# Kernel tuning notes

Measured on AMD Instinct MI355X. Metric: run time of the kernel, lower is better.

The kernel has to match this reference:

```python
import jax, jax.numpy as jnp
import numpy as np

N_NODES = 50000
N_EDGES = 500000
D_IN = 128
D_HID = 128
C = 1.0          # curvature (same for every layer)
MIN_NORM = 1e-15
MAX_TANH_ARG = 15.0
PROJ_EPS = 4e-3  # float32 boundary eps used by hgcn PoincareBall.proj


def _artanh(x):
    x = jnp.clip(x, -1.0 + 1e-7, 1.0 - 1e-7)
    return 0.5 * (jnp.log1p(x) - jnp.log1p(-x))


def _tanh(x):
    return jnp.tanh(jnp.clip(x, -MAX_TANH_ARG, MAX_TANH_ARG))


def _norm(x):
    return jnp.maximum(jnp.linalg.norm(x, axis=-1, keepdims=True), MIN_NORM)


def proj(x, c):
    # clip points to stay strictly inside the Poincare ball
    n = _norm(x)
    maxnorm = (1.0 - PROJ_EPS) / jnp.sqrt(c)
    return jnp.where(n > maxnorm, x / n * maxnorm, x)


def expmap0(u, c):
    sc = jnp.sqrt(c)
    n = _norm(u)
    return _tanh(sc * n) * u / (sc * n)


def logmap0(p, c):
    sc = jnp.sqrt(c)
    n = _norm(p)
    return _artanh(sc * n) * p / (sc * n)


def mobius_add(x, y, c):
    x2 = jnp.sum(x * x, -1, keepdims=True)
    y2 = jnp.sum(y * y, -1, keepdims=True)
    xy = jnp.sum(x * y, -1, keepdims=True)
    num = (1.0 + 2.0 * c * xy + c * y2) * x + (1.0 - c * x2) * y
    den = 1.0 + 2.0 * c * xy + c * c * x2 * y2
    return num / jnp.maximum(den, MIN_NORM)


def mobius_matvec(m, x, c):
    sc = jnp.sqrt(c)
    xn = _norm(x)
    mx = x @ m.T                                   # [N, out]
    mxn = _norm(mx)
    res = _tanh(mxn / xn * _artanh(sc * xn)) * mx / (mxn * sc)
    is_zero = jnp.all(mx == 0.0, axis=-1, keepdims=True)
    return jnp.where(is_zero, jnp.zeros_like(res), res)


def hyp_linear(x, W, b, c):
    h = proj(mobius_matvec(W, x, c), c)
    hyp_bias = proj(expmap0(b[None, :], c), c)     # proj_tan0 is identity on the ball
    return proj(mobius_add(h, hyp_bias, c), c)


def hyp_agg(x, src, dst, edge_weight, c):
    x_tan = logmap0(x, c)                          # [N, d] tangent at origin
    msg = edge_weight[:, None] * x_tan[src]        # [E, d] gather + scale
    agg = jax.ops.segment_sum(msg, dst, num_segments=N_NODES)  # spmm(adj, x_tan)
    return proj(expmap0(agg, c), c)


def hyp_act(x, c_in, c_out):
    xt = jax.nn.relu(logmap0(x, c_in))
    return proj(expmap0(xt, c_out), c_out)


def setup_inputs() -> dict:
    key = jax.random.key(0)
    ks = jax.random.split(key, 8)
    x = jax.random.normal(ks[0], (N_NODES, D_IN), dtype=jnp.float32) * 0.1
    src = jax.random.randint(ks[1], (N_EDGES,), 0, N_NODES)
    dst = jax.random.randint(ks[2], (N_EDGES,), 0, N_NODES)
    edge_weight = jax.random.uniform(ks[3], (N_EDGES,), dtype=jnp.float32) * 0.1
    s1 = 1.0 / np.sqrt(D_IN)
    W1 = jax.random.normal(ks[4], (D_HID, D_IN), dtype=jnp.float32) * s1
    b1 = jax.random.normal(ks[5], (D_HID,), dtype=jnp.float32) * 0.01
    W2 = jax.random.normal(ks[6], (D_HID, D_HID), dtype=jnp.float32) * s1
    b2 = jax.random.normal(ks[7], (D_HID,), dtype=jnp.float32) * 0.01
    return {"x": x, "src": src, "dst": dst, "edge_weight": edge_weight,
            "W1": W1, "b1": b1, "W2": W2, "b2": b2}


def reference(x, src, dst, edge_weight, W1, b1, W2, b2):
    c = jnp.float32(C)
    # HGCN.encode: proj_tan0 (identity for PoincareBall) -> expmap0 -> proj
    h = proj(expmap0(x, c), c)
    # layer 1: HypLinear -> HypAgg -> HypAct
    h = hyp_linear(h, W1, b1, c)
    h = hyp_agg(h, src, dst, edge_weight, c)
    h = hyp_act(h, c, c)
    # layer 2
    h = hyp_linear(h, W2, b2, c)
    h = hyp_agg(h, src, dst, edge_weight, c)
    h = hyp_act(h, c, c)
    return h
```

## Files before the change

### kernel.cpp

```cpp
#include <hip/hip_runtime.h>
#include <math.h>

#define MIN_NORM 1e-15f
#define MAXNORM  0.996f
#define ARTANH_CLIP 0.99999988f

typedef __bf16 bf16x8 __attribute__((ext_vector_type(8)));
typedef float  f32x4  __attribute__((ext_vector_type(4)));

union FragU { ushort u[8]; uint4 q; bf16x8 v; };

__device__ __forceinline__ float wave_sum(float v) {
#pragma unroll
    for (int off = 32; off > 0; off >>= 1) v += __shfl_xor(v, off, 64);
    return v;
}

__device__ __forceinline__ float artanh_c(float x) {
    x = fminf(fmaxf(x, -ARTANH_CLIP), ARTANH_CLIP);
    return 0.5f * (log1pf(x) - log1pf(-x));
}

__device__ __forceinline__ float tanh_c(float x) {
    return tanhf(fminf(fmaxf(x, -15.f), 15.f));
}

__device__ __forceinline__ float proj_factor(float n2) {
    float n = fmaxf(sqrtf(n2), MIN_NORM);
    return (n > MAXNORM) ? (MAXNORM / n) : 1.f;
}

__device__ __forceinline__ unsigned short f2bf(float f) {
    unsigned u = __float_as_uint(f);
    return (unsigned short)((u + 0x7fffu + ((u >> 16) & 1u)) >> 16);
}
__device__ __forceinline__ float bf2f(unsigned short h) {
    return __uint_as_float((unsigned)h << 16);
}
__device__ __forceinline__ float bflo(unsigned u) { return __uint_as_float(u << 16); }
__device__ __forceinline__ float bfhi(unsigned u) { return __uint_as_float(u & 0xffff0000u); }

__device__ __forceinline__ void red16_f4(float4& v) {
#pragma unroll
    for (int off = 1; off < 16; off <<= 1) {
        v.x += __shfl_xor(v.x, off, 64);
        v.y += __shfl_xor(v.y, off, 64);
        v.z += __shfl_xor(v.z, off, 64);
        v.w += __shfl_xor(v.w, off, 64);
    }
}

__device__ __forceinline__ float bcast_row(const float4& v, int r) {
    const int src = (r >> 2) << 4;
    const float a = __shfl(v.x, src, 64);
    const float b = __shfl(v.y, src, 64);
    const float c = __shfl(v.z, src, 64);
    const float d = __shfl(v.w, src, 64);
    const float lo = (r & 1) ? b : a;
    const float hi = (r & 1) ? d : c;
    return (r & 2) ? hi : lo;
}

__device__ __forceinline__ void pack_w4(const float4 w4, int o, int k, char* out) {
    ushort4 h, l;
    h.x = f2bf(w4.x); l.x = f2bf(w4.x - bf2f(h.x));
    h.y = f2bf(w4.y); l.y = f2bf(w4.y - bf2f(h.y));
    h.z = f2bf(w4.z); l.z = f2bf(w4.z - bf2f(h.z));
    h.w = f2bf(w4.w); l.w = f2bf(w4.w - bf2f(h.w));
    const int prow = ((o & 7) << 4) | (o >> 3);
    const unsigned byte = (unsigned)((prow << 8) + (k << 1)) ^ (unsigned)((prow & 7) << 4);
    *reinterpret_cast<ushort4*>(out + byte) = h;
    *reinterpret_cast<ushort4*>(out + 32768 + byte) = l;
}

__global__ __launch_bounds__(256)
void setup_kernel(const float* __restrict__ W1, const float* __restrict__ W2,
                  char* __restrict__ g1, char* __restrict__ g2,
                  const float* __restrict__ b1, const float* __restrict__ b2,
                  float* __restrict__ hb1, float* __restrict__ hb2,
                  const int* __restrict__ dst, int* __restrict__ cnt, int E) {
    const int b = blockIdx.x;
    if (b < 32) {
        const float* W = (b < 16) ? W1 : W2;
        char* out = (b < 16) ? g1 : g2;
        const int i = (((b & 15) * 256) + threadIdx.x) * 4;
        pack_w4(*reinterpret_cast<const float4*>(&W[i]), i >> 7, i & 127, out);
    } else if (b == 32) {
        if (threadIdx.x < 64) {
            const int lane = threadIdx.x;
#pragma unroll
            for (int j = 0; j < 2; ++j) {
                const float* bb = j ? b2 : b1;
                float* hb = j ? hb2 : hb1;
                float v0 = bb[lane], v1 = bb[lane + 64];
                float n2 = wave_sum(v0 * v0 + v1 * v1);
                float n = fmaxf(sqrtf(n2), MIN_NORM);
                float sc = tanh_c(n) / n;
                sc *= proj_factor(sc * sc * n2);
                hb[lane] = v0 * sc;
                hb[lane + 64] = v1 * sc;
            }
        }
    } else {
        const int e = (b - 33) * 256 + threadIdx.x;
        if (e < E) atomicAdd(&cnt[dst[e]], 1);
    }
}


__global__ void scan1(const int* __restrict__ cnt, int* __restrict__ ptr,
                      int* __restrict__ bsum, int N) {
    __shared__ int s[256];
    const int t = threadIdx.x;
    const int i = blockIdx.x * 256 + t;
    int v = (i < N) ? cnt[i] : 0;
    s[t] = v;
    __syncthreads();
#pragma unroll
    for (int off = 1; off < 256; off <<= 1) {
        int add = (t >= off) ? s[t - off] : 0;
        __syncthreads();
        s[t] += add;
        __syncthreads();
    }
    if (i < N) ptr[i] = s[t] - v;
    if (t == 255) bsum[blockIdx.x] = s[255];
}

__global__ void scan2(const int* __restrict__ bsum, int* __restrict__ bscan, int nb) {
    __shared__ int s[256];
    const int t = threadIdx.x;
    int v = (t < nb) ? bsum[t] : 0;
    s[t] = v;
    __syncthreads();
#pragma unroll
    for (int off = 1; off < 256; off <<= 1) {
        int add = (t >= off) ? s[t - off] : 0;
        __syncthreads();
        s[t] += add;
        __syncthreads();
    }
    bscan[t] = s[t] - v;
}

__global__ void scan3(const int* __restrict__ bscan, int* __restrict__ ptr,
                      int* __restrict__ cursor, int N, int E) {
    const int i = blockIdx.x * blockDim.x + threadIdx.x;
    if (i < N) {
        const int p = ptr[i] + bscan[i >> 8];
        ptr[i] = p;
        cursor[i] = p;
    }
    if (i == 0) ptr[N] = E;
}

__global__ void scatter_kernel(const int* __restrict__ src, const int* __restrict__ dst,
                               const float* __restrict__ ew, int* __restrict__ cursor,
                               unsigned* __restrict__ epk, int E) {
    int e = blockIdx.x * blockDim.x + threadIdx.x;
    if (e >= E) return;
    int pos = atomicAdd(&cursor[dst[e]], 1);
    epk[pos] = ((unsigned)src[e] << 16) | (unsigned)f2bf(ew[e]);
}

template <bool PRELUDE, bool BF16IN, bool BF16OUT>
__global__ __launch_bounds__(1024, 4)
void hyp_linear_tan_mfma(const void* __restrict__ xin, const char* __restrict__ gWpack,
                         const float* __restrict__ hb, void* __restrict__ xtan,
                         int n_rows) {
    __shared__ __align__(16) char sW[65536];

    const int tid = threadIdx.x;
    const int lane = tid & 63, wid = tid >> 6;
    const int r15 = lane & 15, g = lane >> 4;

    const int tiles = (n_rows + 15) >> 4;
    const int tile = blockIdx.x + gridDim.x * wid;
    const bool active = (tile < tiles);
    const int rowbase = tile << 4;
    const int myrow = rowbase + r15;
    const bool rok = active && (myrow < n_rows);

    float4 xa[4], xb[4];
    uint4 xu[4];
    if (BF16IN) {
        const char* xr = (const char*)xin + (size_t)myrow * 256 + g * 16;
#pragma unroll
        for (int kc = 0; kc < 4; ++kc)
            xu[kc] = rok ? *reinterpret_cast<const uint4*>(xr + kc * 64)
                         : make_uint4(0u, 0u, 0u, 0u);
    } else {
        const float* xr = (const float*)xin + (size_t)myrow * 128 + g * 8;
#pragma unroll
        for (int kc = 0; kc < 4; ++kc) {
            if (rok) {
                xa[kc] = *reinterpret_cast<const float4*>(xr + kc * 32);
                xb[kc] = *reinterpret_cast<const float4*>(xr + kc * 32 + 4);
            } else {
                xa[kc] = make_float4(0.f, 0.f, 0.f, 0.f);
                xb[kc] = xa[kc];
            }
        }
    }

    {
        const uint4* gsrc = reinterpret_cast<const uint4*>(gWpack);
        uint4* ldst = reinterpret_cast<uint4*>(sW);
#pragma unroll
        for (int i = 0; i < 4; ++i) ldst[tid + i * 1024] = gsrc[tid + i * 1024];
    }

    float yb[8];
    {
        const float4 yba = *reinterpret_cast<const float4*>(&hb[r15 * 8]);
        const float4 ybb = *reinterpret_cast<const float4*>(&hb[r15 * 8 + 4]);
        yb[0] = yba.x; yb[1] = yba.y; yb[2] = yba.z; yb[3] = yba.w;
        yb[4] = ybb.x; yb[5] = ybb.y; yb[6] = ybb.z; yb[7] = ybb.w;
    }
    float y2p = 0.f;
#pragma unroll
    for (int t = 0; t < 8; ++t) y2p += yb[t] * yb[t];
#pragma unroll
    for (int off = 1; off < 16; off <<= 1) y2p += __shfl_xor(y2p, off, 64);
    const float y2 = y2p;

    __syncthreads();
    if (!active) return;

    bf16x8 ah[4], al[4];
    float ss = 0.f;
    if (BF16IN) {
#pragma unroll
        for (int kc = 0; kc < 4; ++kc) {
            FragU fu; fu.q = xu[kc];
            ah[kc] = fu.v;
            const uint4 u = xu[kc];
            float f0 = bflo(u.x), f1 = bfhi(u.x), f2_ = bflo(u.y), f3 = bfhi(u.y);
            float f4 = bflo(u.z), f5 = bfhi(u.z), f6 = bflo(u.w), f7 = bfhi(u.w);
            ss += f0 * f0 + f1 * f1 + f2_ * f2_ + f3 * f3
                + f4 * f4 + f5 * f5 + f6 * f6 + f7 * f7;
        }
    } else {
#pragma unroll
        for (int kc = 0; kc < 4; ++kc) {
            const float4 a = xa[kc], b = xb[kc];
            ss += a.x * a.x + a.y * a.y + a.z * a.z + a.w * a.w
                + b.x * b.x + b.y * b.y + b.z * b.z + b.w * b.w;
            ah[kc][0] = (__bf16)a.x; al[kc][0] = (__bf16)(a.x - (float)ah[kc][0]);
            ah[kc][1] = (__bf16)a.y; al[kc][1] = (__bf16)(a.y - (float)ah[kc][1]);
            ah[kc][2] = (__bf16)a.z; al[kc][2] = (__bf16)(a.z - (float)ah[kc][2]);
            ah[kc][3] = (__bf16)a.w; al[kc][3] = (__bf16)(a.w - (float)ah[kc][3]);
            ah[kc][4] = (__bf16)b.x; al[kc][4] = (__bf16)(b.x - (float)ah[kc][4]);
            ah[kc][5] = (__bf16)b.y; al[kc][5] = (__bf16)(b.y - (float)ah[kc][5]);
            ah[kc][6] = (__bf16)b.z; al[kc][6] = (__bf16)(b.z - (float)ah[kc][6]);
            ah[kc][7] = (__bf16)b.w; al[kc][7] = (__bf16)(b.w - (float)ah[kc][7]);
        }
    }
    ss += __shfl_xor(ss, 16, 64);
    ss += __shfl_xor(ss, 32, 64);

    f32x4 acc[8];
#pragma unroll
    for (int ct = 0; ct < 8; ++ct) acc[ct] = (f32x4){0.f, 0.f, 0.f, 0.f};

    const unsigned lswz = (unsigned)((r15 & 7) << 4);
#pragma unroll
    for (int kc = 0; kc < 4; ++kc) {
#pragma unroll
        for (int ct = 0; ct < 8; ++ct) {
            const unsigned byte =
                ((unsigned)((ct << 12) + (r15 << 8) + (kc << 6) + (g << 4))) ^ lswz;
            FragU bh, bl;
            bh.q = *reinterpret_cast<const uint4*>(sW + byte);
            bl.q = *reinterpret_cast<const uint4*>(sW + 32768 + byte);
            acc[ct] = __builtin_amdgcn_mfma_f32_16x16x32_bf16(ah[kc], bh.v, acc[ct], 0, 0, 0);
            acc[ct] = __builtin_amdgcn_mfma_f32_16x16x32_bf16(ah[kc], bl.v, acc[ct], 0, 0, 0);
            if (!BF16IN)
                acc[ct] = __builtin_amdgcn_mfma_f32_16x16x32_bf16(al[kc], bh.v, acc[ct], 0, 0, 0);
        }
    }

    float4 r2 = make_float4(0.f, 0.f, 0.f, 0.f);
    float4 xyv = make_float4(0.f, 0.f, 0.f, 0.f);
#pragma unroll
    for (int ct = 0; ct < 8; ++ct) {
        r2.x += acc[ct][0] * acc[ct][0];
        r2.y += acc[ct][1] * acc[ct][1];
        r2.z += acc[ct][2] * acc[ct][2];
        r2.w += acc[ct][3] * acc[ct][3];
        xyv.x += acc[ct][0] * yb[ct];
        xyv.y += acc[ct][1] * yb[ct];
        xyv.z += acc[ct][2] * yb[ct];
        xyv.w += acc[ct][3] * yb[ct];
    }
    red16_f4(r2);
    red16_f4(xyv);

    const float rn2 = bcast_row(r2, r15);
    const float xyr = bcast_row(xyv, r15);
    const float n2v = ss;

    const float n = fmaxf(sqrtf(n2v), MIN_NORM);
    float sc = 1.f;
    if (PRELUDE) {
        sc = tanh_c(n) / n;
        sc *= proj_factor(sc * sc * n2v);
    }
    const float xn = fmaxf(sc * n, MIN_NORM);
    const float mxn = fmaxf(sc * sqrtf(rn2), MIN_NORM);
    const float s = tanh_c(mxn / xn * artanh_c(xn));
    const float sl0 = (s * sc) / mxn;
    float m2 = rn2 * sl0 * sl0;
    const float f = proj_factor(m2);
    const float scl = sl0 * f;
    m2 *= f * f;
    const float xy = scl * xyr;
    const float cx = 1.f + 2.f * xy + y2;
    const float cy = 1.f - m2;
    const float rdn = 1.f / fmaxf(1.f + 2.f * xy + m2 * y2, MIN_NORM);
    const float A = cx * scl * rdn;
    const float B = cy * rdn;
    const float on2 = A * A * rn2 + 2.f * A * B * xyr + B * B * y2;
    const float f2 = proj_factor(on2);
    const float onn = fmaxf(sqrtf(on2) * f2, MIN_NORM);
    const float slg = artanh_c(onn) / onn;
    const float P = slg * f2 * A;
    const float Q = slg * f2 * B;

#pragma unroll
    for (int reg = 0; reg < 4; ++reg) {
        const float Pr = __shfl(P, 4 * g + reg, 64);
        const float Qr = __shfl(Q, 4 * g + reg, 64);
        const int row = rowbase + 4 * g + reg;
        if (row < n_rows) {
            float v[8];
#pragma unroll
            for (int ct = 0; ct < 8; ++ct)
                v[ct] = fmaf(Pr, acc[ct][reg], Qr * yb[ct]);
            if (BF16OUT) {
                uint4 pk;
                pk.x = (unsigned)f2bf(v[0]) | ((unsigned)f2bf(v[1]) << 16);
                pk.y = (unsigned)f2bf(v[2]) | ((unsigned)f2bf(v[3]) << 16);
                pk.z = (unsigned)f2bf(v[4]) | ((unsigned)f2bf(v[5]) << 16);
                pk.w = (unsigned)f2bf(v[6]) | ((unsigned)f2bf(v[7]) << 16);
                *reinterpret_cast<uint4*>((char*)xtan + (size_t)row * 256 + r15 * 16) = pk;
            } else {
                float* orow = (float*)xtan + (size_t)row * 128 + r15 * 8;
                *reinterpret_cast<float4*>(orow) = make_float4(v[0], v[1], v[2], v[3]);
                *reinterpret_cast<float4*>(orow + 4) = make_float4(v[4], v[5], v[6], v[7]);
            }
        }
    }
}

template <bool BF16OUT>
__global__ __launch_bounds__(256)
void gather_act(const char* __restrict__ xt, const int* __restrict__ ptr,
                const unsigned* __restrict__ epk, void* __restrict__ out, int n_rows) {
    const int v = blockIdx.x * 4 + (threadIdx.x >> 6);
    if (v >= n_rows) return;
    const int lane = threadIdx.x & 63;
    const int q = lane >> 4, t = lane & 15;
    const char* xtl = xt + (t << 4);
    const int beg = ptr[v], end = ptr[v + 1];

    float acc[8];
#pragma unroll
    for (int j = 0; j < 8; ++j) acc[j] = 0.f;

    unsigned p = (beg + q < end) ? epk[beg + q] : 0u;
    for (int i = beg; i < end; i += 4) {
        const unsigned rowoff = (p & 0xffff0000u) >> 8;
        const uint4 u = *reinterpret_cast<const uint4*>(xtl + rowoff);
        const int en = i + 4 + q;
        const unsigned pn = (en < end) ? epk[en] : 0u;
        const float w = __uint_as_float(p << 16);
        acc[0] = fmaf(w, bflo(u.x), acc[0]);
        acc[1] = fmaf(w, bfhi(u.x), acc[1]);
        acc[2] = fmaf(w, bflo(u.y), acc[2]);
        acc[3] = fmaf(w, bfhi(u.y), acc[3]);
        acc[4] = fmaf(w, bflo(u.z), acc[4]);
        acc[5] = fmaf(w, bfhi(u.z), acc[5]);
        acc[6] = fmaf(w, bflo(u.w), acc[6]);
        acc[7] = fmaf(w, bfhi(u.w), acc[7]);
        p = pn;
    }

#pragma unroll
    for (int j = 0; j < 8; ++j) {
        acc[j] += __shfl_xor(acc[j], 16, 64);
        acc[j] += __shfl_xor(acc[j], 32, 64);
    }

    float s = 0.f;
#pragma unroll
    for (int j = 0; j < 8; ++j) s += acc[j] * acc[j];
#pragma unroll
    for (int off = 1; off < 16; off <<= 1) s += __shfl_xor(s, off, 64);
    const float n2 = s;

    float n = fmaxf(sqrtf(n2), MIN_NORM);
    float sc = tanh_c(n) / n;
    float hn2 = sc * sc * n2;
    float f = proj_factor(hn2);
    sc *= f; hn2 *= f * f;
    float hn = fmaxf(sqrtf(hn2), MIN_NORM);
    float sl = artanh_c(hn) / hn;
    const float scl1 = sc * sl;

    float x[8];
    float s2 = 0.f;
#pragma unroll
    for (int j = 0; j < 8; ++j) {
        x[j] = fmaxf(acc[j] * scl1, 0.f);
        s2 += x[j] * x[j];
    }
#pragma unroll
    for (int off = 1; off < 16; off <<= 1) s2 += __shfl_xor(s2, off, 64);
    float nb = fmaxf(sqrtf(s2), MIN_NORM);
    float scb = tanh_c(nb) / nb;
    scb *= proj_factor(scb * scb * s2);

    const float o0 = x[2 * q] * scb, o1 = x[2 * q + 1] * scb;
    if (BF16OUT) {
        const unsigned pk = (unsigned)f2bf(o0) | ((unsigned)f2bf(o1) << 16);
        *reinterpret_cast<unsigned*>((char*)out + (size_t)v * 256 + t * 16 + q * 4) = pk;
    } else {
        *reinterpret_cast<float2*>((float*)out + (size_t)v * 128 + t * 8 + q * 2) =
            make_float2(o0, o1);
    }
}

__global__ __launch_bounds__(256)
void agg_edges(const float* __restrict__ xtan, const int* __restrict__ src,
               const int* __restrict__ dst, const float* __restrict__ ew,
               float* __restrict__ agg, int n_edges) {
    int gt = blockIdx.x * blockDim.x + threadIdx.x;
    int e = gt >> 5;
    if (e >= n_edges) return;
    int c = (gt & 31) << 2;
    int sN = src[e], dN = dst[e];
    float w = ew[e];
    const float4 v = *reinterpret_cast<const float4*>(&xtan[(size_t)sN * 128 + c]);
    float* ap = &agg[(size_t)dN * 128 + c];
    atomicAdd(ap + 0, w * v.x);
    atomicAdd(ap + 1, w * v.y);
    atomicAdd(ap + 2, w * v.z);
    atomicAdd(ap + 3, w * v.w);
}

__global__ __launch_bounds__(256)
void hyp_act_kernel(const float* __restrict__ in, float* __restrict__ out, int n_rows) {
    int row = blockIdx.x * 4 + (threadIdx.x >> 6);
    if (row >= n_rows) return;
    int lane = threadIdx.x & 63;
    int l2 = lane << 1;
    const float2 v = *reinterpret_cast<const float2*>(&in[(size_t)row * 128 + l2]);
    float a0 = v.x, a1 = v.y;
    float n2 = wave_sum(a0 * a0 + a1 * a1);
    float n = fmaxf(sqrtf(n2), MIN_NORM);
    float sc = tanh_c(n) / n;
    float hn2 = sc * sc * n2;
    float f = proj_factor(hn2);
    sc *= f; hn2 *= f * f;
    float h0 = a0 * sc, h1 = a1 * sc;
    float hn = fmaxf(sqrtf(hn2), MIN_NORM);
    float sl = artanh_c(hn) / hn;
    float x0 = fmaxf(h0 * sl, 0.f), x1 = fmaxf(h1 * sl, 0.f);
    float n2b = wave_sum(x0 * x0 + x1 * x1);
    float nb = fmaxf(sqrtf(n2b), MIN_NORM);
    float scb = tanh_c(nb) / nb;
    scb *= proj_factor(scb * scb * n2b);
    *reinterpret_cast<float2*>(&out[(size_t)row * 128 + l2]) =
        make_float2(x0 * scb, x1 * scb);
}

__global__ void bias_kernel(const float* __restrict__ b1, const float* __restrict__ b2,
                            float* __restrict__ hb1, float* __restrict__ hb2) {
    int lane = threadIdx.x;
#pragma unroll
    for (int j = 0; j < 2; ++j) {
        const float* b = j ? b2 : b1;
        float* hb = j ? hb2 : hb1;
        float v0 = b[lane], v1 = b[lane + 64];
        float n2 = wave_sum(v0 * v0 + v1 * v1);
        float n = fmaxf(sqrtf(n2), MIN_NORM);
        float sc = tanh_c(n) / n;
        sc *= proj_factor(sc * sc * n2);
        hb[lane] = v0 * sc;
        hb[lane + 64] = v1 * sc;
    }
}

__global__ void prep_w(const float* __restrict__ W1, const float* __restrict__ W2,
                       char* __restrict__ g1, char* __restrict__ g2) {
    const int b = blockIdx.x;
    const float* W = (b < 16) ? W1 : W2;
    char* out = (b < 16) ? g1 : g2;
    const int i = (((b & 15) * 256) + threadIdx.x) * 4;
    pack_w4(*reinterpret_cast<const float4*>(&W[i]), i >> 7, i & 127, out);
}

extern "C" void kernel_launch(void* const* d_in, const int* in_sizes, int n_in,
                              void* d_out, int out_size, void* d_ws, size_t ws_size,
                              hipStream_t stream) {
    const float* x   = (const float*)d_in[0];
    const int*   src = (const int*)d_in[1];
    const int*   dst = (const int*)d_in[2];
    const float* ew  = (const float*)d_in[3];
    const float* W1  = (const float*)d_in[4];
    const float* b1  = (const float*)d_in[5];
    const float* W2  = (const float*)d_in[6];
    const float* b2  = (const float*)d_in[7];

    const int N = in_sizes[0] / 128;
    const int E = in_sizes[1];
    float* fout = (float*)d_out;

    const int tiles = (N + 15) >> 4;
    int lin_grid = 256;
    while (lin_grid * 16 < tiles) lin_grid += 256;
    const int nbE = (E + 255) / 256;
    const int nbN = (N + 255) / 256;

    const size_t need = 131072 + 1024
                      + (size_t)N * 256 * 2
                      + (size_t)E * 4
                      + ((size_t)(N + 1) + N + N + 512) * 4;

    if (ws_size >= need) {
        char*  base  = (char*)d_ws;
        char*  gW1p  = base;
        char*  gW2p  = base + 65536;
        float* hb1   = (float*)(base + 131072);
        float* hb2   = hb1 + 128;
        char*  xtA   = base + 131072 + 1024;
        char*  xtB   = xtA + (size_t)N * 256;
        unsigned* epk = (unsigned*)(xtB + (size_t)N * 256);
        int* ptr     = (int*)(epk + E);
        int* cnt     = ptr + (N + 1);
        int* cursor  = cnt + N;
        int* bsum    = cursor + N;
        int* bscan   = bsum + 256;

        hipMemsetAsync(cnt, 0, (size_t)N * 4, stream);
        setup_kernel<<<33 + nbE, 256, 0, stream>>>(W1, W2, gW1p, gW2p,
                                                   b1, b2, hb1, hb2, dst, cnt, E);
        scan1<<<nbN, 256, 0, stream>>>(cnt, ptr, bsum, N);
        scan2<<<1, 256, 0, stream>>>(bsum, bscan, nbN);
        scan3<<<nbN, 256, 0, stream>>>(bscan, ptr, cursor, N, E);
        scatter_kernel<<<nbE, 256, 0, stream>>>(src, dst, ew, cursor, epk, E);

        hyp_linear_tan_mfma<true, false, true><<<lin_grid, 1024, 0, stream>>>(x, gW1p, hb1, xtA, N);
        gather_act<true><<<(N + 3) / 4, 256, 0, stream>>>(xtA, ptr, epk, xtB, N);
        hyp_linear_tan_mfma<false, true, true><<<lin_grid, 1024, 0, stream>>>(xtB, gW2p, hb2, xtA, N);
        gather_act<false><<<(N + 3) / 4, 256, 0, stream>>>(xtA, ptr, epk, fout, N);
    } else {
        char*  gW1p = (char*)d_ws;
        char*  gW2p = gW1p + 65536;
        float* hb1  = (float*)(gW2p + 65536);
        float* hb2  = hb1 + 128;
        float* nbuf = hb2 + 128;
        const size_t node_bytes = (size_t)N * 128 * sizeof(float);
        const int agg_blocks = (int)(((size_t)E * 32 + 255) / 256);
        const int row_blocks = (N + 3) / 4;

        prep_w<<<32, 256, 0, stream>>>(W1, W2, gW1p, gW2p);
        bias_kernel<<<1, 64, 0, stream>>>(b1, b2, hb1, hb2);
        hyp_linear_tan_mfma<true, false, false><<<lin_grid, 1024, 0, stream>>>(x, gW1p, hb1, fout, N);
        hipMemsetAsync(nbuf, 0, node_bytes, stream);
        agg_edges<<<agg_blocks, 256, 0, stream>>>(fout, src, dst, ew, nbuf, E);
        hyp_act_kernel<<<row_blocks, 256, 0, stream>>>(nbuf, nbuf, N);
        hyp_linear_tan_mfma<false, false, false><<<lin_grid, 1024, 0, stream>>>(nbuf, gW2p, hb2, fout, N);
        hipMemsetAsync(fout, 0, node_bytes, stream);
        agg_edges<<<agg_blocks, 256, 0, stream>>>(fout, src, dst, ew, nbuf, E);
        hyp_act_kernel<<<row_blocks, 256, 0, stream>>>(nbuf, fout, N);
    }
}
```

Measured before the change: 194.9 us.

## Fuse CSR scan into one block, pad segments, fast transcendentals, smaller linear blocks

Replaces the three-kernel prefix scan with a single 1024-thread block kernel, and pads each destination's edge list to a multiple of four using zeroed entries. The gather loop can then drop its bounds checks. It also swaps the precise tanh, artanh and log1p calls for __expf/__logf based approximations. The hyperbolic linear kernel now uses 512-thread blocks with a contiguous tile mapping, so each block loads the weight tile into shared memory for only 8 tiles. The trade-offs are lower accuracy near the ball boundary, a serial single-block scan, and more weight reloads into shared memory.

```diff
diff --git a/kernel.cpp b/kernel.cpp
--- a/kernel.cpp
+++ b/kernel.cpp
@@ -16,13 +16,13 @@
     return v;
 }
 
-__device__ __forceinline__ float artanh_c(float x) {
-    x = fminf(fmaxf(x, -ARTANH_CLIP), ARTANH_CLIP);
-    return 0.5f * (log1pf(x) - log1pf(-x));
-}
-
-__device__ __forceinline__ float tanh_c(float x) {
-    return tanhf(fminf(fmaxf(x, -15.f), 15.f));
+__device__ __forceinline__ float tanh_fast(float x) {
+    const float t = __expf(2.f * fminf(x, 15.f));
+    return 1.f - 2.f / (t + 1.f);
+}
+__device__ __forceinline__ float artanh_fast(float x) {
+    x = fminf(x, ARTANH_CLIP);
+    return 0.5f * __logf((1.f + x) / (1.f - x));
 }
 
 __device__ __forceinline__ float proj_factor(float n2) {
@@ -95,7 +95,7 @@
                 float v0 = bb[lane], v1 = bb[lane + 64];
                 float n2 = wave_sum(v0 * v0 + v1 * v1);
                 float n = fmaxf(sqrtf(n2), MIN_NORM);
-                float sc = tanh_c(n) / n;
+                float sc = tanh_fast(n) / n;
                 sc *= proj_factor(sc * sc * n2);
                 hb[lane] = v0 * sc;
                 hb[lane + 64] = v1 * sc;
@@ -107,51 +107,33 @@
     }
 }
 
-
-__global__ void scan1(const int* __restrict__ cnt, int* __restrict__ ptr,
-                      int* __restrict__ bsum, int N) {
-    __shared__ int s[256];
+__global__ __launch_bounds__(1024)
+void scan_fused(const int* __restrict__ cnt, int* __restrict__ ptr,
+                int* __restrict__ cursor, int N) {
+    __shared__ int s[1024];
     const int t = threadIdx.x;
-    const int i = blockIdx.x * 256 + t;
-    int v = (i < N) ? cnt[i] : 0;
-    s[t] = v;
+    const int C = (N + 1023) >> 10;
+    const int i0 = t * C;
+    const int i1 = min(i0 + C, N);
+    int sum = 0;
+    for (int i = i0; i < i1; ++i) sum += (cnt[i] + 3) & ~3;
+    s[t] = sum;
     __syncthreads();
 #pragma unroll
-    for (int off = 1; off < 256; off <<= 1) {
+    for (int off = 1; off < 1024; off <<= 1) {
         int add = (t >= off) ? s[t - off] : 0;
         __syncthreads();
         s[t] += add;
         __syncthreads();
     }
-    if (i < N) ptr[i] = s[t] - v;
-    if (t == 255) bsum[blockIdx.x] = s[255];
-}
-
-__global__ void scan2(const int* __restrict__ bsum, int* __restrict__ bscan, int nb) {
-    __shared__ int s[256];
-    const int t = threadIdx.x;
-    int v = (t < nb) ? bsum[t] : 0;
-    s[t] = v;
-    __syncthreads();
-#pragma unroll
-    for (int off = 1; off < 256; off <<= 1) {
-        int add = (t >= off) ? s[t - off] : 0;
-        __syncthreads();
-        s[t] += add;
-        __syncthreads();
-    }
-    bscan[t] = s[t] - v;
-}
-
-__global__ void scan3(const int* __restrict__ bscan, int* __restrict__ ptr,
-                      int* __restrict__ cursor, int N, int E) {
-    const int i = blockIdx.x * blockDim.x + threadIdx.x;
-    if (i < N) {
-        const int p = ptr[i] + bscan[i >> 8];
-        ptr[i] = p;
-        cursor[i] = p;
-    }
-    if (i == 0) ptr[N] = E;
+    int run = s[t] - sum;
+    for (int i = i0; i < i1; ++i) {
+        const int pc = (cnt[i] + 3) & ~3;
+        ptr[i] = run;
+        cursor[i] = run;
+        run += pc;
+    }
+    if (t == 1023) ptr[N] = s[1023];
 }
 
 __global__ void scatter_kernel(const int* __restrict__ src, const int* __restrict__ dst,
@@ -164,7 +146,7 @@
 }
 
 template <bool PRELUDE, bool BF16IN, bool BF16OUT>
-__global__ __launch_bounds__(1024, 4)
+__global__ __launch_bounds__(512, 4)
 void hyp_linear_tan_mfma(const void* __restrict__ xin, const char* __restrict__ gWpack,
                          const float* __restrict__ hb, void* __restrict__ xtan,
                          int n_rows) {
@@ -175,7 +157,7 @@
     const int r15 = lane & 15, g = lane >> 4;
 
     const int tiles = (n_rows + 15) >> 4;
-    const int tile = blockIdx.x + gridDim.x * wid;
+    const int tile = blockIdx.x * 8 + wid;
     const bool active = (tile < tiles);
     const int rowbase = tile << 4;
     const int myrow = rowbase + r15;
@@ -207,7 +189,7 @@
         const uint4* gsrc = reinterpret_cast<const uint4*>(gWpack);
         uint4* ldst = reinterpret_cast<uint4*>(sW);
 #pragma unroll
-        for (int i = 0; i < 4; ++i) ldst[tid + i * 1024] = gsrc[tid + i * 1024];
+        for (int i = 0; i < 8; ++i) ldst[tid + i * 512] = gsrc[tid + i * 512];
     }
 
     float yb[8];
@@ -303,12 +285,12 @@
     const float n = fmaxf(sqrtf(n2v), MIN_NORM);
     float sc = 1.f;
     if (PRELUDE) {
-        sc = tanh_c(n) / n;
+        sc = tanh_fast(n) / n;
         sc *= proj_factor(sc * sc * n2v);
     }
     const float xn = fmaxf(sc * n, MIN_NORM);
     const float mxn = fmaxf(sc * sqrtf(rn2), MIN_NORM);
-    const float s = tanh_c(mxn / xn * artanh_c(xn));
+    const float s = tanh_fast(mxn / xn * artanh_fast(xn));
     const float sl0 = (s * sc) / mxn;
     float m2 = rn2 * sl0 * sl0;
     const float f = proj_factor(m2);
@@ -323,7 +305,7 @@
     const float on2 = A * A * rn2 + 2.f * A * B * xyr + B * B * y2;
     const float f2 = proj_factor(on2);
     const float onn = fmaxf(sqrtf(on2) * f2, MIN_NORM);
-    const float slg = artanh_c(onn) / onn;
+    const float slg = artanh_fast(onn) / onn;
     const float P = slg * f2 * A;
     const float Q = slg * f2 * B;
 
@@ -362,18 +344,18 @@
     const int lane = threadIdx.x & 63;
     const int q = lane >> 4, t = lane & 15;
     const char* xtl = xt + (t << 4);
-    const int beg = ptr[v], end = ptr[v + 1];
+    const int beg = ptr[v];
+    const int it = (ptr[v + 1] - beg) >> 2;
 
     float acc[8];
 #pragma unroll
     for (int j = 0; j < 8; ++j) acc[j] = 0.f;
 
-    unsigned p = (beg + q < end) ? epk[beg + q] : 0u;
-    for (int i = beg; i < end; i += 4) {
-        const unsigned rowoff = (p & 0xffff0000u) >> 8;
-        const uint4 u = *reinterpret_cast<const uint4*>(xtl + rowoff);
-        const int en = i + 4 + q;
-        const unsigned pn = (en < end) ? epk[en] : 0u;
+    const unsigned* ep = epk + beg + q;
+    unsigned p = (it > 0) ? ep[0] : 0u;
+    for (int k = 1; k <= it; ++k) {
+        const uint4 u = *reinterpret_cast<const uint4*>(xtl + ((p >> 16) << 8));
+        const unsigned pn = ep[k * 4];
         const float w = __uint_as_float(p << 16);
         acc[0] = fmaf(w, bflo(u.x), acc[0]);
         acc[1] = fmaf(w, bfhi(u.x), acc[1]);
@@ -400,12 +382,12 @@
     const float n2 = s;
 
     float n = fmaxf(sqrtf(n2), MIN_NORM);
-    float sc = tanh_c(n) / n;
+    float sc = tanh_fast(n) / n;
     float hn2 = sc * sc * n2;
     float f = proj_factor(hn2);
     sc *= f; hn2 *= f * f;
     float hn = fmaxf(sqrtf(hn2), MIN_NORM);
-    float sl = artanh_c(hn) / hn;
+    float sl = artanh_fast(hn) / hn;
     const float scl1 = sc * sl;
 
     float x[8];
@@ -418,7 +400,7 @@
 #pragma unroll
     for (int off = 1; off < 16; off <<= 1) s2 += __shfl_xor(s2, off, 64);
     float nb = fmaxf(sqrtf(s2), MIN_NORM);
-    float scb = tanh_c(nb) / nb;
+    float scb = tanh_fast(nb) / nb;
     scb *= proj_factor(scb * scb * s2);
 
     const float o0 = x[2 * q] * scb, o1 = x[2 * q + 1] * scb;
@@ -459,17 +441,17 @@
     float a0 = v.x, a1 = v.y;
     float n2 = wave_sum(a0 * a0 + a1 * a1);
     float n = fmaxf(sqrtf(n2), MIN_NORM);
-    float sc = tanh_c(n) / n;
+    float sc = tanh_fast(n) / n;
     float hn2 = sc * sc * n2;
     float f = proj_factor(hn2);
     sc *= f; hn2 *= f * f;
     float h0 = a0 * sc, h1 = a1 * sc;
     float hn = fmaxf(sqrtf(hn2), MIN_NORM);
-    float sl = artanh_c(hn) / hn;
+    float sl = artanh_fast(hn) / hn;
     float x0 = fmaxf(h0 * sl, 0.f), x1 = fmaxf(h1 * sl, 0.f);
     float n2b = wave_sum(x0 * x0 + x1 * x1);
     float nb = fmaxf(sqrtf(n2b), MIN_NORM);
-    float scb = tanh_c(nb) / nb;
+    float scb = tanh_fast(nb) / nb;
     scb *= proj_factor(scb * scb * n2b);
     *reinterpret_cast<float2*>(&out[(size_t)row * 128 + l2]) =
         make_float2(x0 * scb, x1 * scb);
@@ -485,7 +467,7 @@
         float v0 = b[lane], v1 = b[lane + 64];
         float n2 = wave_sum(v0 * v0 + v1 * v1);
         float n = fmaxf(sqrtf(n2), MIN_NORM);
-        float sc = tanh_c(n) / n;
+        float sc = tanh_fast(n) / n;
         sc *= proj_factor(sc * sc * n2);
         hb[lane] = v0 * sc;
         hb[lane + 64] = v1 * sc;
@@ -518,15 +500,16 @@
     float* fout = (float*)d_out;
 
     const int tiles = (N + 15) >> 4;
-    int lin_grid = 256;
-    while (lin_grid * 16 < tiles) lin_grid += 256;
+    const int lin_grid = (tiles + 7) / 8;
     const int nbE = (E + 255) / 256;
-    const int nbN = (N + 255) / 256;
+
+    const size_t epk_words = (size_t)E + 3 * (size_t)N + 16;
 
     const size_t need = 131072 + 1024
                       + (size_t)N * 256 * 2
-                      + (size_t)E * 4
-                      + ((size_t)(N + 1) + N + N + 512) * 4;
+                      + (epk_words + N) * 4
+                      + ((size_t)(N + 1) + N) * 4
+                      + 1024;
 
     if (ws_size >= need) {
         char*  base  = (char*)d_ws;
@@ -537,23 +520,19 @@
         char*  xtA   = base + 131072 + 1024;
         char*  xtB   = xtA + (size_t)N * 256;
         unsigned* epk = (unsigned*)(xtB + (size_t)N * 256);
-        int* ptr     = (int*)(epk + E);
-        int* cnt     = ptr + (N + 1);
-        int* cursor  = cnt + N;
-        int* bsum    = cursor + N;
-        int* bscan   = bsum + 256;
-
-        hipMemsetAsync(cnt, 0, (size_t)N * 4, stream);
+        int* cnt     = (int*)(epk + epk_words);
+        int* ptr     = cnt + N;
+        int* cursor  = ptr + (N + 1);
+
+        hipMemsetAsync(epk, 0, (epk_words + N) * 4, stream);
         setup_kernel<<<33 + nbE, 256, 0, stream>>>(W1, W2, gW1p, gW2p,
                                                    b1, b2, hb1, hb2, dst, cnt, E);
-        scan1<<<nbN, 256, 0, stream>>>(cnt, ptr, bsum, N);
-        scan2<<<1, 256, 0, stream>>>(bsum, bscan, nbN);
-        scan3<<<nbN, 256, 0, stream>>>(bscan, ptr, cursor, N, E);
+        scan_fused<<<1, 1024, 0, stream>>>(cnt, ptr, cursor, N);
         scatter_kernel<<<nbE, 256, 0, stream>>>(src, dst, ew, cursor, epk, E);
 
-        hyp_linear_tan_mfma<true, false, true><<<lin_grid, 1024, 0, stream>>>(x, gW1p, hb1, xtA, N);
+        hyp_linear_tan_mfma<true, false, true><<<lin_grid, 512, 0, stream>>>(x, gW1p, hb1, xtA, N);
         gather_act<true><<<(N + 3) / 4, 256, 0, stream>>>(xtA, ptr, epk, xtB, N);
-        hyp_linear_tan_mfma<false, true, true><<<lin_grid, 1024, 0, stream>>>(xtB, gW2p, hb2, xtA, N);
+        hyp_linear_tan_mfma<false, true, true><<<lin_grid, 512, 0, stream>>>(xtB, gW2p, hb2, xtA, N);
         gather_act<false><<<(N + 3) / 4, 256, 0, stream>>>(xtA, ptr, epk, fout, N);
     } else {
         char*  gW1p = (char*)d_ws;
@@ -567,11 +546,11 @@
 
         prep_w<<<32, 256, 0, stream>>>(W1, W2, gW1p, gW2p);
         bias_kernel<<<1, 64, 0, stream>>>(b1, b2, hb1, hb2);
-        hyp_linear_tan_mfma<true, false, false><<<lin_grid, 1024, 0, stream>>>(x, gW1p, hb1, fout, N);
+        hyp_linear_tan_mfma<true, false, false><<<lin_grid, 512, 0, stream>>>(x, gW1p, hb1, fout, N);
         hipMemsetAsync(nbuf, 0, node_bytes, stream);
         agg_edges<<<agg_blocks, 256, 0, stream>>>(fout, src, dst, ew, nbuf, E);
         hyp_act_kernel<<<row_blocks, 256, 0, stream>>>(nbuf, nbuf, N);
-        hyp_linear_tan_mfma<false, false, false><<<lin_grid, 1024, 0, stream>>>(nbuf, gW2p, hb2, fout, N);
+        hyp_linear_tan_mfma<false, false, false><<<lin_grid, 512, 0, stream>>>(nbuf, gW2p, hb2, fout, N);
         hipMemsetAsync(fout, 0, node_bytes, stream);
         agg_edges<<<agg_blocks, 256, 0, stream>>>(fout, src, dst, ew, nbuf, E);
         hyp_act_kernel<<<row_blocks, 256, 0, stream>>>(nbuf, fout, N);
```

New measurement: 269.1 us. +38.1%, slower.
